# Performance work log

Hardware: AMD Instinct MI355X
Metric: run time of the kernel (lower is better)

Reference implementation:

```python
import jax, jax.numpy as jnp
import numpy as np

W_SEG = 2048   # segment length w
R = 4          # dilation rate
OFFSET = 0     # offset < r
H = 16         # num heads
C = 1024       # embed dim
M = W_SEG // R # tokens attended per segment


def _mha(xi, w_in, b_in, w_out, b_out):
    # xi: (b, s, m, c) -> causal multi-head self-attention per segment
    b, s, m, c = xi.shape
    dh = c // H
    qkv = jnp.einsum('bsmc,ec->bsme', xi, w_in) + b_in  # e = 3c
    q, k, v = jnp.split(qkv, 3, axis=-1)
    q = q.reshape(b, s, m, H, dh)
    k = k.reshape(b, s, m, H, dh)
    v = v.reshape(b, s, m, H, dh)
    scores = jnp.einsum('bsqhd,bskhd->bshqk', q, k) / jnp.sqrt(jnp.asarray(dh, xi.dtype))
    causal = jnp.tril(jnp.ones((m, m), dtype=bool))
    scores = jnp.where(causal, scores, jnp.asarray(-1e9, xi.dtype))
    p = jax.nn.softmax(scores, axis=-1)
    o = jnp.einsum('bshqk,bskhd->bsqhd', p, v).reshape(b, s, m, c)
    return jnp.einsum('bsmc,oc->bsmo', o, w_out) + b_out


def setup_inputs() -> dict:
    key = jax.random.key(0)
    k1, k2, k3, k4, k5 = jax.random.split(key, 5)
    x = jax.random.normal(k1, (4, 8192, C), dtype=jnp.float32)
    w_in = jax.random.normal(k2, (3 * C, C), dtype=jnp.float32) * (C ** -0.5)
    b_in = jnp.zeros((3 * C,), dtype=jnp.float32)
    w_out = jax.random.normal(k3, (C, C), dtype=jnp.float32) * (C ** -0.5)
    b_out = jnp.zeros((C,), dtype=jnp.float32)
    return {"x": x, "w_in": w_in, "b_in": b_in, "w_out": w_out, "b_out": b_out}


def reference(x, w_in, b_in, w_out, b_out):
    b, n, c = x.shape
    s = n // W_SEG  # number of segments
    xr = x.reshape(b, s, W_SEG, c)
    xi = xr[:, :, OFFSET::R, :]                # (b, s, m, c) dilated gather
    oi = _mha(xi, w_in, b_in, w_out, b_out)    # attention per segment
    out = jnp.zeros_like(xr).at[:, :, OFFSET::R, :].set(oi)  # scatter (disjoint indices)
    return out.reshape(b, n, c)
```

## Files before the change

### kernel.cpp

```cpp
#include <hip/hip_runtime.h>


typedef unsigned short u16;
typedef short short8 __attribute__((ext_vector_type(8)));
typedef short short4v __attribute__((ext_vector_type(4)));
typedef float f32x4 __attribute__((ext_vector_type(4)));

__device__ __forceinline__ u16 f2bf(float f) {
  unsigned u = __builtin_bit_cast(unsigned, f);
  u += 0x7FFFu + ((u >> 16) & 1u);
  return (u16)(u >> 16);
}

__device__ __forceinline__ void gload_lds16(const void* g, void* l) {
  __builtin_amdgcn_global_load_lds((const __attribute__((address_space(1))) void*)g,
                                   (__attribute__((address_space(3))) void*)l,
                                   16, 0, 0);
}

#define SBAR() asm volatile("s_barrier" ::: "memory")

__global__ void conv_gather(const float* __restrict__ x, u16* __restrict__ xi) {
  int t = blockIdx.x * 256 + threadIdx.x;
  if (t >= (8192 * 1024) / 8) return;
  int row = t >> 7;
  int col = (t & 127) << 3;
  size_t src = ((size_t)((row >> 9) << 11) + ((row & 511) << 2)) * 1024 + col;
  float4 v0 = *(const float4*)(x + src);
  float4 v1 = *(const float4*)(x + src + 4);
  short8 o;
  o[0] = f2bf(v0.x); o[1] = f2bf(v0.y); o[2] = f2bf(v0.z); o[3] = f2bf(v0.w);
  o[4] = f2bf(v1.x); o[5] = f2bf(v1.y); o[6] = f2bf(v1.z); o[7] = f2bf(v1.w);
  *(short8*)(xi + (size_t)row * 1024 + col) = o;
}

__global__ void conv_plain(const float* __restrict__ in, u16* __restrict__ out, int n8) {
  int t = blockIdx.x * 256 + threadIdx.x;
  if (t >= n8) return;
  size_t base = (size_t)t * 8;
  float4 v0 = *(const float4*)(in + base);
  float4 v1 = *(const float4*)(in + base + 4);
  short8 o;
  o[0] = f2bf(v0.x); o[1] = f2bf(v0.y); o[2] = f2bf(v0.z); o[3] = f2bf(v0.w);
  o[4] = f2bf(v1.x); o[5] = f2bf(v1.y); o[6] = f2bf(v1.z); o[7] = f2bf(v1.w);
  *(short8*)(out + base) = o;
}

template <int NCOLS, int MODE>
__global__ __launch_bounds__(512) void gemm_pipe(
    const u16* __restrict__ A, const u16* __restrict__ B,
    const float* __restrict__ bias, void* __restrict__ Cout) {
  constexpr int K = 1024, NT = 16, NTILE = NCOLS / 256;
  __shared__ u16 lds[3][24576];

  const int tid = threadIdx.x;
  const int w = tid >> 6, lane = tid & 63;
  const int wm = w >> 2, wn = w & 3;
  const int g = lane >> 4, lq = lane & 15;

  const int per = gridDim.x >> 3;
  const int s = (blockIdx.x & 7) * per + (blockIdx.x >> 3);
  const int m0 = (s / NTILE) * 128, n0 = (s % NTILE) * 256;

  const int srow = w * 8 + (lane >> 3);
  const int jch = (lane & 7) ^ ((lane >> 3) & 7);
  const u16* Ab = A + (size_t)(m0 + srow) * K + jch * 8;
  const u16* Bb = B + (size_t)(n0 + srow) * K + jch * 8;
  const int ldst = w * 512 + lane * 8;

#define SA(buf_, qd, kt) gload_lds16(Ab + (size_t)(qd) * 64 * K + (kt) * 64, &lds[buf_][(qd) * 4096 + ldst])
#define SB(buf_, qd, kt) gload_lds16(Bb + (size_t)(qd) * 64 * K + (kt) * 64, &lds[buf_][8192 + (qd) * 4096 + ldst])

  const int xw = lq & 7;
  const int arow = wm * 64 + lq;
  const int brow = wn * 64 + lq;

#define RDA(dst_, kc)                                                             \
  _Pragma("unroll") for (int mi = 0; mi < 4; ++mi)                                \
      dst_[mi] = *(const short8*)(&lds[buf][(arow + mi * 16) * 64 + (((kc) * 4 + g) ^ xw) * 8]);
#define RDB(dst_, kc)                                                             \
  _Pragma("unroll") for (int ni = 0; ni < 4; ++ni)                                \
      dst_[ni] = *(const short8*)(&lds[buf][8192 + (brow + ni * 16) * 64 + (((kc) * 4 + g) ^ xw) * 8]);

  f32x4 acc[4][4] = {};

  SA(0, 0, 0); SA(0, 1, 0); SB(0, 0, 0); SB(0, 1, 0); SB(0, 2, 0); SB(0, 3, 0);
  SA(1, 0, 1); SA(1, 1, 1); SB(1, 0, 1); SB(1, 1, 1); SB(1, 2, 1); SB(1, 3, 1);
  asm volatile("s_waitcnt vmcnt(6)" ::: "memory");
  SBAR();

#pragma unroll 1
  for (int t = 0; t < NT; ++t) {
    const int buf = t % 3, nb = (t + 2) % 3;
    short8 a0[4], b0[4], a1[4], b1[4];

    if (t + 2 < NT) {
      SA(nb, 0, t + 2); SA(nb, 1, t + 2);
      SB(nb, 0, t + 2); SB(nb, 1, t + 2); SB(nb, 2, t + 2); SB(nb, 3, t + 2);
    }
    RDA(a0, 0); RDB(b0, 0); RDA(a1, 1); RDB(b1, 1);
    if (t + 2 < NT) { asm volatile("s_waitcnt vmcnt(6)" ::: "memory"); }
    else            { asm volatile("s_waitcnt vmcnt(0)" ::: "memory"); }
    SBAR();
    __builtin_amdgcn_s_setprio(1);
#pragma unroll
    for (int mi = 0; mi < 4; ++mi)
#pragma unroll
      for (int ni = 0; ni < 4; ++ni)
        acc[mi][ni] = __builtin_amdgcn_mfma_f32_16x16x32_bf16(a0[mi], b0[ni], acc[mi][ni], 0, 0, 0);
#pragma unroll
    for (int mi = 0; mi < 4; ++mi)
#pragma unroll
      for (int ni = 0; ni < 4; ++ni)
        acc[mi][ni] = __builtin_amdgcn_mfma_f32_16x16x32_bf16(a1[mi], b1[ni], acc[mi][ni], 0, 0, 0);
    __builtin_amdgcn_s_setprio(0);
    SBAR();
  }

  if (MODE == 0) {
    u16* C = (u16*)Cout;
    if (n0 < 2048) {
#pragma unroll
      for (int mi = 0; mi < 4; ++mi) {
#pragma unroll
        for (int ni = 0; ni < 4; ++ni) {
          const int col = n0 + wn * 64 + ni * 16 + lq;
          const float bv = bias[col];
          u16* dst = C + (size_t)(col >> 10) * 8388608 + (col & 1023);
#pragma unroll
          for (int r = 0; r < 4; ++r) {
            const int m = m0 + wm * 64 + mi * 16 + g * 4 + r;
            dst[(size_t)m * 1024] = f2bf(acc[mi][ni][r] + bv);
          }
        }
      }
    } else {
      u16* vt = C + 16777216;
#pragma unroll
      for (int mi = 0; mi < 4; ++mi) {
        const int m4 = m0 + wm * 64 + mi * 16 + g * 4;
        const int bs = m4 >> 9, k = m4 & 511;
#pragma unroll
        for (int ni = 0; ni < 4; ++ni) {
          const int cv = n0 - 2048 + wn * 64 + ni * 16 + lq;
          const int h = cv >> 6, d = cv & 63;
          const float bv = bias[cv + 2048];
          short4v pk;
#pragma unroll
          for (int r = 0; r < 4; ++r) pk[r] = (short)f2bf(acc[mi][ni][r] + bv);
          *(short4v*)(&vt[(size_t)((bs * 16 + h) * 64 + d) * 512 + k]) = pk;
        }
      }
    }
  } else {
    float* O = (float*)Cout;
#pragma unroll
    for (int mi = 0; mi < 4; ++mi) {
#pragma unroll
      for (int ni = 0; ni < 4; ++ni) {
        const int col = n0 + wn * 64 + ni * 16 + lq;
        const float bv = bias[col];
#pragma unroll
        for (int r = 0; r < 4; ++r) {
          const int m = m0 + wm * 64 + mi * 16 + g * 4 + r;
          const int orow = ((m >> 9) << 11) + ((m & 511) << 2);
          O[(size_t)orow * 1024 + col] = acc[mi][ni][r] + bv;
        }
      }
    }
    for (int i = 0; i < 48; ++i) {
      const int idx = i * 512 + tid;
      const int z = idx >> 13;
      const int mm = (idx & 8191) >> 6;
      const int ch = idx & 63;
      const int m = m0 + mm;
      const int orow = ((m >> 9) << 11) + ((m & 511) << 2) + 1 + z;
      *(float4*)(O + (size_t)orow * 1024 + n0 + ch * 4) =
          make_float4(0.f, 0.f, 0.f, 0.f);
    }
  }
#undef SA
#undef SB
#undef RDA
#undef RDB
}

__global__ __launch_bounds__(512) void attn_kernel(const u16* __restrict__ qkv,
                                                   u16* __restrict__ o_ws) {
  __shared__ u16 Ks[512 * 64];
  __shared__ u16 Vs[64 * 512];
  __shared__ u16 Pl[8][16][40];

  const int tid = threadIdx.x;
  const int w = tid >> 6, lane = tid & 63;
  const int g = lane >> 4, lq = lane & 15;
  const int bh = blockIdx.x;
  const int bs = bh >> 4, h = bh & 15;

  const u16* baseq = qkv + (size_t)bs * 512 * 1024 + h * 64;
  const u16* basek = qkv + 8388608 + (size_t)bs * 512 * 1024 + h * 64;
  const u16* vhead = qkv + 16777216 + (size_t)bh * 32768;

  {
    const int rsub = lane >> 3;
    const int csw = (lane & 7) ^ rsub;
#pragma unroll
    for (int i = 0; i < 8; ++i) {
      const int step = i * 8 + w;
      gload_lds16(basek + (size_t)(step * 8 + rsub) * 1024 + csw * 8,
                  &Ks[step * 512 + lane * 8]);
    }
#pragma unroll
    for (int i = 0; i < 8; ++i) {
      const int d = i * 8 + w;
      gload_lds16(vhead + (size_t)d * 512 + (lane ^ (d & 7)) * 8,
                  &Vs[d * 512 + lane * 8]);
    }
  }
  __syncthreads();

  const int xw = lq & 7;
#pragma unroll 1
  for (int qi = 0; qi < 4; ++qi) {
    const int qt = ((qi & 1) ? (15 - w) : w) + (qi >> 1) * 16;
    const int q0 = qt * 16;
    const short8 qf0 = *(const short8*)(baseq + (size_t)(q0 + lq) * 1024 + g * 8);
    const short8 qf1 = *(const short8*)(baseq + (size_t)(q0 + lq) * 1024 + 32 + g * 8);
    f32x4 oacc[4] = {};
    float l_r[4] = {0.f, 0.f, 0.f, 0.f};
    const int nst = (qt + 2) >> 1;
#pragma unroll 1
    for (int kk = 0; kk < nst; ++kk) {
      const int kb = kk * 32;
      const bool last = (kk == nst - 1);
      f32x4 s[2];
#pragma unroll
      for (int tt = 0; tt < 2; ++tt) {
        const int r = kb + tt * 16 + lq;
        short8 klo = *(const short8*)(&Ks[r * 64 + ((g ^ xw) * 8)]);
        short8 khi = *(const short8*)(&Ks[r * 64 + (((4 + g) ^ xw) * 8)]);
        f32x4 z = {};
        z = __builtin_amdgcn_mfma_f32_16x16x32_bf16(qf0, klo, z, 0, 0, 0);
        z = __builtin_amdgcn_mfma_f32_16x16x32_bf16(qf1, khi, z, 0, 0, 0);
        s[tt] = z;
      }
#pragma unroll
      for (int tt = 0; tt < 2; ++tt) {
#pragma unroll
        for (int r = 0; r < 4; ++r) {
          float p = __expf(s[tt][r] * 0.125f);
          if (last && (kb + tt * 16 + lq > q0 + g * 4 + r)) p = 0.f;
          l_r[r] += p;
          Pl[w][g * 4 + r][tt * 16 + lq] = f2bf(p);
        }
      }
      short8 pf = *(const short8*)(&Pl[w][lq][g * 8]);
#pragma unroll
      for (int dt = 0; dt < 4; ++dt) {
        const int vr = dt * 16 + lq;
        short8 vf = *(const short8*)(&Vs[vr * 512 + ((((kb >> 3) + g) ^ xw) * 8)]);
        oacc[dt] = __builtin_amdgcn_mfma_f32_16x16x32_bf16(pf, vf, oacc[dt], 0, 0, 0);
      }
    }
#pragma unroll
    for (int r = 0; r < 4; ++r) {
      float l = l_r[r];
      l += __shfl_xor(l, 1);
      l += __shfl_xor(l, 2);
      l += __shfl_xor(l, 4);
      l += __shfl_xor(l, 8);
      const float inv = 1.0f / l;
      const int q = q0 + g * 4 + r;
      u16* dst = o_ws + (size_t)(bs * 512 + q) * 1024 + h * 64;
#pragma unroll
      for (int dt = 0; dt < 4; ++dt) dst[dt * 16 + lq] = f2bf(oacc[dt][r] * inv);
    }
  }
}

extern "C" void kernel_launch(void* const* d_in, const int* in_sizes, int n_in,
                              void* d_out, int out_size, void* d_ws, size_t ws_size,
                              hipStream_t stream) {
  const float* x     = (const float*)d_in[0];
  const float* w_in  = (const float*)d_in[1];
  const float* b_in  = (const float*)d_in[2];
  const float* w_out = (const float*)d_in[3];
  const float* b_out = (const float*)d_in[4];

  char* ws = (char*)d_ws;
  u16* xi_bf   = (u16*)(ws);
  u16* win_bf  = (u16*)(ws + 16777216);
  u16* wout_bf = (u16*)(ws + 16777216 + 6291456);
  u16* qkv     = (u16*)(ws + 16777216 + 6291456 + 2097152);
  u16* o_bf    = (u16*)(ws + 16777216 + 6291456 + 2097152 + 50331648);

  conv_gather<<<4096, 256, 0, stream>>>(x, xi_bf);
  conv_plain<<<1536, 256, 0, stream>>>(w_in, win_bf, (3072 * 1024) / 8);
  conv_plain<<<512, 256, 0, stream>>>(w_out, wout_bf, (1024 * 1024) / 8);
  gemm_pipe<3072, 0><<<768, 512, 0, stream>>>(xi_bf, win_bf, b_in, qkv);
  attn_kernel<<<256, 512, 0, stream>>>(qkv, o_bf);
  gemm_pipe<1024, 1><<<256, 512, 0, stream>>>(o_bf, wout_bf, b_out, d_out);
}
```

Before: 147.8 us.

## Double-buffer LDS fragment reads in GEMM to overlap with MFMA

```diff
diff --git a/kernel.cpp b/kernel.cpp
--- a/kernel.cpp
+++ b/kernel.cpp
@@ -70,51 +70,60 @@
 
 #define SA(buf_, qd, kt) gload_lds16(Ab + (size_t)(qd) * 64 * K + (kt) * 64, &lds[buf_][(qd) * 4096 + ldst])
 #define SB(buf_, qd, kt) gload_lds16(Bb + (size_t)(qd) * 64 * K + (kt) * 64, &lds[buf_][8192 + (qd) * 4096 + ldst])
+#define STAGE6(kt)                                                                 \
+  { const int nb_ = (kt) % 3;                                                      \
+    SA(nb_, 0, kt); SA(nb_, 1, kt);                                                \
+    SB(nb_, 0, kt); SB(nb_, 1, kt); SB(nb_, 2, kt); SB(nb_, 3, kt); }
 
   const int xw = lq & 7;
   const int arow = wm * 64 + lq;
   const int brow = wn * 64 + lq;
 
-#define RDA(dst_, kc)                                                             \
-  _Pragma("unroll") for (int mi = 0; mi < 4; ++mi)                                \
-      dst_[mi] = *(const short8*)(&lds[buf][(arow + mi * 16) * 64 + (((kc) * 4 + g) ^ xw) * 8]);
-#define RDB(dst_, kc)                                                             \
-  _Pragma("unroll") for (int ni = 0; ni < 4; ++ni)                                \
-      dst_[ni] = *(const short8*)(&lds[buf][8192 + (brow + ni * 16) * 64 + (((kc) * 4 + g) ^ xw) * 8]);
+#define READ_TILE(aset, bset, tile_)                                               \
+  { const int bufr = (tile_) % 3;                                                  \
+    _Pragma("unroll") for (int kc = 0; kc < 2; ++kc) {                             \
+      _Pragma("unroll") for (int mi = 0; mi < 4; ++mi)                             \
+        aset[mi + 4 * kc] = *(const short8*)(                                      \
+            &lds[bufr][(arow + mi * 16) * 64 + ((kc * 4 + g) ^ xw) * 8]);          \
+      _Pragma("unroll") for (int ni = 0; ni < 4; ++ni)                             \
+        bset[ni + 4 * kc] = *(const short8*)(                                      \
+            &lds[bufr][8192 + (brow + ni * 16) * 64 + ((kc * 4 + g) ^ xw) * 8]);   \
+    } }
+
+#define MFMA_TILE(aset, bset)                                                      \
+  __builtin_amdgcn_s_setprio(1);                                                   \
+  _Pragma("unroll") for (int kc = 0; kc < 2; ++kc)                                 \
+    _Pragma("unroll") for (int mi = 0; mi < 4; ++mi)                               \
+      _Pragma("unroll") for (int ni = 0; ni < 4; ++ni)                             \
+        acc[mi][ni] = __builtin_amdgcn_mfma_f32_16x16x32_bf16(                     \
+            aset[mi + 4 * kc], bset[ni + 4 * kc], acc[mi][ni], 0, 0, 0);           \
+  __builtin_amdgcn_s_setprio(0);
 
   f32x4 acc[4][4] = {};
-
-  SA(0, 0, 0); SA(0, 1, 0); SB(0, 0, 0); SB(0, 1, 0); SB(0, 2, 0); SB(0, 3, 0);
-  SA(1, 0, 1); SA(1, 1, 1); SB(1, 0, 1); SB(1, 1, 1); SB(1, 2, 1); SB(1, 3, 1);
+  short8 aA[8], bA[8], aB[8], bB[8];
+
+  STAGE6(0); STAGE6(1);
   asm volatile("s_waitcnt vmcnt(6)" ::: "memory");
   SBAR();
+  READ_TILE(aA, bA, 0);
 
 #pragma unroll 1
-  for (int t = 0; t < NT; ++t) {
-    const int buf = t % 3, nb = (t + 2) % 3;
-    short8 a0[4], b0[4], a1[4], b1[4];
-
-    if (t + 2 < NT) {
-      SA(nb, 0, t + 2); SA(nb, 1, t + 2);
-      SB(nb, 0, t + 2); SB(nb, 1, t + 2); SB(nb, 2, t + 2); SB(nb, 3, t + 2);
-    }
-    RDA(a0, 0); RDB(b0, 0); RDA(a1, 1); RDB(b1, 1);
-    if (t + 2 < NT) { asm volatile("s_waitcnt vmcnt(6)" ::: "memory"); }
-    else            { asm volatile("s_waitcnt vmcnt(0)" ::: "memory"); }
+  for (int tt = 0; tt < NT; tt += 2) {
+    if (tt + 2 < NT) STAGE6(tt + 2);
+    if (tt + 2 < NT) { asm volatile("s_waitcnt vmcnt(6)" ::: "memory"); }
+    else             { asm volatile("s_waitcnt vmcnt(0)" ::: "memory"); }
+    asm volatile("s_waitcnt lgkmcnt(0)" ::: "memory");
     SBAR();
-    __builtin_amdgcn_s_setprio(1);
-#pragma unroll
-    for (int mi = 0; mi < 4; ++mi)
-#pragma unroll
-      for (int ni = 0; ni < 4; ++ni)
-        acc[mi][ni] = __builtin_amdgcn_mfma_f32_16x16x32_bf16(a0[mi], b0[ni], acc[mi][ni], 0, 0, 0);
-#pragma unroll
-    for (int mi = 0; mi < 4; ++mi)
-#pragma unroll
-      for (int ni = 0; ni < 4; ++ni)
-        acc[mi][ni] = __builtin_amdgcn_mfma_f32_16x16x32_bf16(a1[mi], b1[ni], acc[mi][ni], 0, 0, 0);
-    __builtin_amdgcn_s_setprio(0);
+    READ_TILE(aB, bB, tt + 1);
+    MFMA_TILE(aA, bA);
+
+    if (tt + 3 < NT) STAGE6(tt + 3);
+    if (tt + 3 < NT) { asm volatile("s_waitcnt vmcnt(6)" ::: "memory"); }
+    else             { asm volatile("s_waitcnt vmcnt(0)" ::: "memory"); }
+    asm volatile("s_waitcnt lgkmcnt(0)" ::: "memory");
     SBAR();
+    if (tt + 2 < NT) READ_TILE(aA, bA, tt + 2);
+    MFMA_TILE(aB, bB);
   }
 
   if (MODE == 0) {
@@ -181,8 +190,9 @@
   }
 #undef SA
 #undef SB
-#undef RDA
-#undef RDB
+#undef STAGE6
+#undef READ_TILE
+#undef MFMA_TILE
 }
 
 __global__ __launch_bounds__(512) void attn_kernel(const u16* __restrict__ qkv,
```

Result: faster. 139.1 us (-5.9%).
